# Kernel tuning notes

Hardware: AMD Instinct MI355X
Metric: run time of the kernel (lower is better)

The kernel has to match this reference:

```python
import jax, jax.numpy as jnp
import numpy as np

N_NODES = 50000
N_EDGES = 800000
F = 53
B = 128
H = 4


def _p(key, shape, scale=0.1):
    return jax.random.normal(key, shape, dtype=jnp.float32) * scale


def setup_inputs() -> dict:
    key = jax.random.key(0)
    ks = jax.random.split(key, 40)
    inp = {
        'x': jax.random.normal(ks[0], (N_NODES, F), dtype=jnp.float32),
        'edge_index': jax.random.randint(ks[1], (2, N_EDGES), 0, N_NODES),
        'batch': jnp.sort(jax.random.randint(ks[2], (N_NODES,), 0, B)),
        # GATConv(53 -> 53, heads=4)
        'gat_w': _p(ks[3], (F, H * F)),
        'gat_att_src': _p(ks[4], (H, F)),
        'gat_att_dst': _p(ks[5], (H, F)),
        'gat_bias': _p(ks[6], (H * F,)),
        # GINConv MLP: 53 -> 106 -> 106
        'gin_w1': _p(ks[7], (F, 2 * F)), 'gin_b1': _p(ks[8], (2 * F,)),
        'gin_w2': _p(ks[9], (2 * F, 2 * F)), 'gin_b2': _p(ks[10], (2 * F,)),
        # EdgeConv MLP: 106 -> 106 -> 106
        'ec_w1': _p(ks[11], (2 * F, 2 * F)), 'ec_b1': _p(ks[12], (2 * F,)),
        'ec_w2': _p(ks[13], (2 * F, 2 * F)), 'ec_b2': _p(ks[14], (2 * F,)),
        # per-branch heads
        'fg1_w': _p(ks[15], (4 * F, 256)), 'fg1_b': _p(ks[16], (256,)),
        'fg2_w': _p(ks[17], (256, 128)), 'fg2_b': _p(ks[18], (128,)),
        'fg3_w': _p(ks[19], (2 * F, 256)), 'fg3_b': _p(ks[20], (256,)),
        'fg4_w': _p(ks[21], (256, 128)), 'fg4_b': _p(ks[22], (128,)),
        'fg5_w': _p(ks[23], (2 * F, 256)), 'fg5_b': _p(ks[24], (256,)),
        'fg6_w': _p(ks[25], (256, 128)), 'fg6_b': _p(ks[26], (128,)),
        # final MLP
        'fc1_w': _p(ks[27], (384, 128)), 'fc1_b': _p(ks[28], (128,)),
        'fc2_w': _p(ks[29], (128, 64)), 'fc2_b': _p(ks[30], (64,)),
        'out_w': _p(ks[31], (64, 1)), 'out_b': _p(ks[32], (1,)),
    }
    return inp


def _gat(x, src, dst, w, a_src, a_dst, bias):
    # PyG GATConv with add_self_loops=True, negative_slope=0.2, concat heads
    n = x.shape[0]
    loop = jnp.arange(n)
    s = jnp.concatenate([src, loop])
    d = jnp.concatenate([dst, loop])
    xh = (x @ w).reshape(n, H, F)                      # [N,H,F]
    al_s = jnp.einsum('nhf,hf->nh', xh, a_src)         # [N,H]
    al_d = jnp.einsum('nhf,hf->nh', xh, a_dst)
    e = jax.nn.leaky_relu(al_s[s] + al_d[d], 0.2)      # [E2,H]
    m = jax.ops.segment_max(e, d, num_segments=n)
    ex = jnp.exp(e - m[d])
    z = jax.ops.segment_sum(ex, d, num_segments=n)
    alpha = ex / (z[d] + 1e-16)                        # softmax over in-edges
    msg = xh[s] * alpha[:, :, None]                    # [E2,H,F]
    out = jax.ops.segment_sum(msg, d, num_segments=n)
    return out.reshape(n, H * F) + bias


def _gin(x, src, dst, w1, b1, w2, b2):
    # PyG GINConv, eps=0: nn(x + sum_j x_j)
    n = x.shape[0]
    agg = jax.ops.segment_sum(x[src], dst, num_segments=n)
    h = x + agg
    return jax.nn.relu(h @ w1 + b1) @ w2 + b2


def _edgeconv(x, src, dst, w1, b1, w2, b2):
    # PyG EdgeConv: max_j nn([x_i, x_j - x_i]) at target i
    n = x.shape[0]
    xi = x[dst]
    feat = jnp.concatenate([xi, x[src] - xi], axis=-1)  # [E,2F]
    h = jax.nn.relu(feat @ w1 + b1) @ w2 + b2
    out = jax.ops.segment_max(h, dst, num_segments=n)
    return jnp.where(jnp.isfinite(out), out, 0.0)       # empty segments -> 0


def _gep(x, batch):
    # global mean pool per graph
    s = jax.ops.segment_sum(x, batch, num_segments=B)
    cnt = jax.ops.segment_sum(jnp.ones((x.shape[0],), x.dtype), batch, num_segments=B)
    return s / jnp.maximum(cnt, 1.0)[:, None]


def reference(x, edge_index, batch,
              gat_w, gat_att_src, gat_att_dst, gat_bias,
              gin_w1, gin_b1, gin_w2, gin_b2,
              ec_w1, ec_b1, ec_w2, ec_b2,
              fg1_w, fg1_b, fg2_w, fg2_b, fg3_w, fg3_b,
              fg4_w, fg4_b, fg5_w, fg5_b, fg6_w, fg6_b,
              fc1_w, fc1_b, fc2_w, fc2_b, out_w, out_b):
    relu = jax.nn.relu
    src, dst = edge_index[0], edge_index[1]

    xt = relu(_gat(x, src, dst, gat_w, gat_att_src, gat_att_dst, gat_bias))
    xt = _gep(xt, batch)
    xt = relu(xt @ fg1_w + fg1_b)
    xt = relu(xt @ fg2_w + fg2_b)

    xt2 = relu(_gin(x, src, dst, gin_w1, gin_b1, gin_w2, gin_b2))
    xt2 = _gep(xt2, batch)
    xt2 = relu(xt2 @ fg3_w + fg3_b)
    xt2 = relu(xt2 @ fg4_w + fg4_b)

    xt3 = relu(_edgeconv(x, src, dst, ec_w1, ec_b1, ec_w2, ec_b2))
    xt3 = _gep(xt3, batch)
    xt3 = relu(xt3 @ fg5_w + fg5_b)
    xt3 = relu(xt3 @ fg6_w + fg6_b)

    h = jnp.concatenate([xt, xt2, xt3], axis=1)         # [B,384]
    h = relu(h @ fc1_w + fc1_b)
    h = relu(h @ fc2_w + fc2_b)
    return jax.nn.sigmoid(h @ out_w + out_b)            # [B,1]
```

## Files before the change

kernel.cpp:

```cpp
#include <hip/hip_runtime.h>
#include <hip/hip_bf16.h>
#include <math.h>

#define N_NODES 50000
#define N_EDGES 800000
#define FDIM 53
#define BATCH 128
#define HF 212
#define F2 106
#define POOLW 424
#define PSTR 32
#define ECS 128
#define A4P 256

typedef __attribute__((ext_vector_type(8))) short short8;
typedef __attribute__((ext_vector_type(4))) float f32x4;

__device__ __forceinline__ float leaky02(float x){ return x >= 0.f ? x : 0.2f * x; }

__device__ __forceinline__ short f2bf(float x) {
  unsigned u = __float_as_uint(x);
  unsigned r = (u + 0x7fffu + ((u >> 16) & 1u)) >> 16;
  return (short)r;
}
__device__ __forceinline__ float bf2f(short b) {
  return __uint_as_float(((unsigned)(unsigned short)b) << 16);
}
__device__ __forceinline__ unsigned pk2(float a, float b) {
  union { __hip_bfloat162 h; unsigned u; } c;
  c.h = __float22bfloat162_rn(make_float2(a, b));
  return c.u;
}
__device__ __forceinline__ void ldsbar() {
  __builtin_amdgcn_s_waitcnt(0xC07F);
  __builtin_amdgcn_s_barrier();
}

#define SEG_CAL 424
#define SEG_WGT (4*56*64)
#define SEG_WUV (2*112*256)
#define SEG_WG1 (112*128)
#define SEG_WG2 (112*128)
#define PREP_TOT (SEG_CAL + SEG_WGT + SEG_WUV + SEG_WG1 + SEG_WG2)
__global__ void k_prep(const float* __restrict__ gat_w, const float* __restrict__ asrc,
                       const float* __restrict__ adst, const float* __restrict__ ec_w1,
                       const float* __restrict__ gin_w1, const float* __restrict__ gin_w2,
                       float* __restrict__ cAl, short* __restrict__ Wgt,
                       short* __restrict__ Wuv, short* __restrict__ Wg1,
                       short* __restrict__ Wg2) {
  int idx = blockIdx.x * blockDim.x + threadIdx.x;
  if (idx < SEG_CAL) {
    int k = idx >> 3, r = idx & 7, sd = r >> 2, h = r & 3;
    const float* av = sd ? adst : asrc;
    float acc = 0.f;
    for (int f = 0; f < FDIM; ++f)
      acc += gat_w[k * HF + h * FDIM + f] * av[h * FDIM + f];
    cAl[idx] = acc;
    return;
  }
  idx -= SEG_CAL;
  if (idx < SEG_WGT) {
    int h = idx / (56 * 64), rem = idx % (56 * 64);
    int n = rem >> 6, kk = rem & 63;
    Wgt[idx] = (kk < FDIM && n < FDIM) ? f2bf(gat_w[kk * HF + h * FDIM + n]) : (short)0;
    return;
  }
  idx -= SEG_WGT;
  if (idx < SEG_WUV) {
    int c = idx / (112 * 256), rem = idx % (112 * 256);
    int n = rem >> 8, kk = rem & 255, ks = kk & 63;
    float w = 0.f;
    if (ks < FDIM && n < F2)
      w = (c == 0) ? ec_w1[ks * F2 + n] - ec_w1[(FDIM + ks) * F2 + n]
                   : ec_w1[(FDIM + ks) * F2 + n];
    short hv = f2bf(w);
    Wuv[idx] = (kk < 128) ? hv : f2bf(w - bf2f(hv));
    return;
  }
  idx -= SEG_WUV;
  if (idx < SEG_WG1) {
    int n = idx >> 7, kk = idx & 127, ks = kk & 63;
    Wg1[idx] = (ks < FDIM && n < F2) ? f2bf(gin_w1[ks * F2 + n]) : (short)0;
    return;
  }
  idx -= SEG_WG1;
  if (idx < SEG_WG2) {
    int n = idx >> 7, kk = idx & 127;
    Wg2[idx] = (kk < F2 && n < F2) ? f2bf(gin_w2[kk * F2 + n]) : (short)0;
  }
}

__global__ __launch_bounds__(256) void k_xsplit(
    const float* __restrict__ x, const float* __restrict__ cAl,
    short* __restrict__ xbhl, float* __restrict__ alS, float* __restrict__ alD) {
  int wid = threadIdx.x >> 6, lane = threadIdx.x & 63;
  int i = blockIdx.x * 4 + wid;
  if (i >= N_NODES) return;
  float v = (lane < FDIM) ? x[(size_t)i * FDIM + lane] : 0.f;
  short hi = f2bf(v);
  xbhl[(size_t)i * 128 + lane] = hi;
  xbhl[(size_t)i * 128 + 64 + lane] = f2bf(v - bf2f(hi));
  float out = 0.f;
#pragma unroll
  for (int j = 0; j < 8; j++) {
    float p = (lane < FDIM) ? v * cAl[lane * 8 + j] : 0.f;
#pragma unroll
    for (int off = 32; off >= 1; off >>= 1) p += __shfl_xor(p, off);
    if (lane == j) out = p;
  }
  if (lane < 4) alS[i * 4 + lane] = out;
  else if (lane < 8) alD[i * 4 + (lane - 4)] = out;
}

__global__ __launch_bounds__(256) void k_uv(
    const short* __restrict__ xbhl, const short* __restrict__ Wuv,
    const float* __restrict__ ec_b1,
    short* __restrict__ Ub, short* __restrict__ Vb) {
  int bid = blockIdx.x;
  int nb = bid >> 1, c = bid & 1;
  int m0 = nb * 64;
  int t = threadIdx.x;
  const int lane = t & 63, wid = t >> 6;
  const int n16 = lane & 15, quad = lane >> 4;
  const int mrow0 = wid * 16;
  const size_t abase = (size_t)(m0 + mrow0 + n16) * 128;
  short8 a[4];
#pragma unroll
  for (int f = 0; f < 4; f++)
    a[f] = *(const short8*)(xbhl + abase + f * 32 + quad * 8);
  const short* Bw = Wuv + (size_t)c * 112 * 256;
  short* Ob = c ? Vb : Ub;
#pragma unroll
  for (int nt = 0; nt < 7; nt++) {
    f32x4 acc = {0.f, 0.f, 0.f, 0.f};
#pragma unroll
    for (int f = 0; f < 8; f++) {
      short8 bf = *(const short8*)(Bw + (nt * 16 + n16) * 256 + f * 32 + quad * 8);
      acc = __builtin_amdgcn_mfma_f32_16x16x32_bf16(a[f & 3], bf, acc, 0, 0, 0);
    }
    int jn = nt * 16 + n16;
    if (jn < F2) {
      float bj = c ? 0.f : ec_b1[jn];
#pragma unroll
      for (int r = 0; r < 4; r++) {
        int gm = m0 + mrow0 + quad * 4 + r;
        if (gm < N_NODES) Ob[(size_t)gm * ECS + jn] = f2bf(acc[r] + bj);
      }
    }
  }
}

#define SCAN_BLOCKS ((N_NODES + 255) / 256)

__global__ void k_hist(const int* __restrict__ ei, int* __restrict__ histP) {
  int t = blockIdx.x * blockDim.x + threadIdx.x;
  if (t < N_EDGES) atomicAdd(&histP[ei[N_EDGES + t] << 5], 1);
}

__global__ __launch_bounds__(256) void k_scan1(const int* __restrict__ histP,
                                               const int* __restrict__ batch,
                                               int* __restrict__ rp, int* __restrict__ bsum,
                                               int* __restrict__ start) {
  __shared__ int buf[256];
  int tid = threadIdx.x;
  int idx = blockIdx.x * 256 + tid;
  int v = (idx < N_NODES) ? histP[idx << 5] : 0;
  buf[tid] = v;
  __syncthreads();
  for (int off = 1; off < 256; off <<= 1) {
    int t2 = (tid >= off) ? buf[tid - off] : 0;
    __syncthreads();
    buf[tid] += t2;
    __syncthreads();
  }
  if (idx < N_NODES) rp[idx] = buf[tid] - v;
  if (tid == 255) bsum[blockIdx.x] = buf[255];
  if (idx < N_NODES) {
    int b = batch[idx];
    if (idx == 0)
      for (int g = 0; g <= b; g++) start[g] = 0;
    int bn = (idx + 1 < N_NODES) ? batch[idx + 1] : BATCH;
    for (int g = b + 1; g <= bn; g++) start[g] = idx + 1;
  }
}

__global__ __launch_bounds__(256) void k_scan3(const int* __restrict__ bsum,
                                               int* __restrict__ rp, int* __restrict__ histP) {
  __shared__ int buf[256];
  int tid = threadIdx.x;
  int v = (tid < SCAN_BLOCKS) ? bsum[tid] : 0;
  buf[tid] = v;
  __syncthreads();
  for (int off = 1; off < 256; off <<= 1) {
    int t2 = (tid >= off) ? buf[tid - off] : 0;
    __syncthreads();
    buf[tid] += t2;
    __syncthreads();
  }
  int boff = (blockIdx.x == 0) ? 0 : buf[blockIdx.x - 1];
  int idx = blockIdx.x * 256 + tid;
  if (idx < N_NODES) {
    int o = rp[idx] + boff;
    rp[idx] = o;
    histP[idx << 5] = o;
  }
  if (idx == 0) rp[N_NODES] = N_EDGES;
}

__global__ void k_scatter(const int* __restrict__ ei, int* __restrict__ histP,
                          int* __restrict__ colidx) {
  int e = blockIdx.x * blockDim.x + threadIdx.x;
  if (e >= N_EDGES) return;
  int d = ei[N_EDGES + e];
  int pos = atomicAdd(&histP[d << 5], 1);
  colidx[pos] = ei[e];
}

#define GCH 20
__global__ __launch_bounds__(256) void k_gatgin(
    const short* __restrict__ xbhl, const float* __restrict__ alS, const float* __restrict__ alD,
    const int* __restrict__ rp, const int* __restrict__ colidx,
    short* __restrict__ agg4, short* __restrict__ aggb) {
  int wid = threadIdx.x >> 6, lane = threadIdx.x & 63;
  bool fa = lane < FDIM;
  int i0 = blockIdx.x * GCH;
  int iend = min(i0 + GCH, N_NODES);
  __shared__ int rpG[GCH + 1];
  __shared__ int sL[4][64];
  __shared__ float4 eL[4][64];
  {
    int t = threadIdx.x, nn = iend - i0;
    if (t <= nn) rpG[t] = rp[i0 + t];
  }
  __syncthreads();
  for (int i = i0 + wid; i < iend; i += 4) {
    int base = rpG[i - i0], deg = rpG[i - i0 + 1] - base;
    float4 adv = *(const float4*)(alD + (size_t)i * 4);
    float4 asv = *(const float4*)(alS + (size_t)i * 4);
    float aldi[4] = {adv.x, adv.y, adv.z, adv.w};
    float exs[4];
    exs[0] = __expf(leaky02(asv.x + aldi[0]));
    exs[1] = __expf(leaky02(asv.y + aldi[1]));
    exs[2] = __expf(leaky02(asv.z + aldi[2]));
    exs[3] = __expf(leaky02(asv.w + aldi[3]));
    float xiv = fa ? bf2f(xbhl[(size_t)i * 128 + lane]) : 0.f;
    float ag0 = exs[0] * xiv, ag1 = exs[1] * xiv, ag2 = exs[2] * xiv, ag3 = exs[3] * xiv;
    float ax = xiv;
    float zl[4] = {0.f, 0.f, 0.f, 0.f};

    for (int c0 = 0; c0 < deg; c0 += 64) {
      int cn = min(64, deg - c0);
      int s = 0;
      float ex0 = 0.f, ex1 = 0.f, ex2 = 0.f, ex3 = 0.f;
      if (lane < cn) {
        s = colidx[base + c0 + lane];
        float4 av = *(const float4*)(alS + (size_t)s * 4);
        ex0 = __expf(leaky02(av.x + aldi[0]));
        ex1 = __expf(leaky02(av.y + aldi[1]));
        ex2 = __expf(leaky02(av.z + aldi[2]));
        ex3 = __expf(leaky02(av.w + aldi[3]));
        zl[0] += ex0; zl[1] += ex1; zl[2] += ex2; zl[3] += ex3;
      }
      sL[wid][lane] = s;
      eL[wid][lane] = make_float4(ex0, ex1, ex2, ex3);
      for (int jj = 0; jj < cn; jj += 4) {
        int4 s4 = *(const int4*)&sL[wid][jj];
        int sj[4] = {s4.x, s4.y, s4.z, s4.w};
        float4 e0 = eL[wid][jj + 0];
        float4 e1 = eL[wid][jj + 1];
        float4 e2 = eL[wid][jj + 2];
        float4 e3 = eL[wid][jj + 3];
        float xg[4];
#pragma unroll
        for (int q = 0; q < 4; q++)
          xg[q] = fa ? bf2f(xbhl[(size_t)sj[q] * 128 + lane]) : 0.f;
        ag0 += e0.x * xg[0] + e1.x * xg[1] + e2.x * xg[2] + e3.x * xg[3];
        ag1 += e0.y * xg[0] + e1.y * xg[1] + e2.y * xg[2] + e3.y * xg[3];
        ag2 += e0.z * xg[0] + e1.z * xg[1] + e2.z * xg[2] + e3.z * xg[3];
        ag3 += e0.w * xg[0] + e1.w * xg[1] + e2.w * xg[2] + e3.w * xg[3];
#pragma unroll
        for (int q = 0; q < 4; q++)
          if (jj + q < cn) ax += xg[q];
      }
    }
#pragma unroll
    for (int off = 32; off >= 1; off >>= 1)
#pragma unroll
      for (int h = 0; h < 4; h++) zl[h] += __shfl_xor(zl[h], off);
    {
      float z0 = zl[0] + exs[0] + 1e-16f;
      float z1 = zl[1] + exs[1] + 1e-16f;
      float z2 = zl[2] + exs[2] + 1e-16f;
      float z3 = zl[3] + exs[3] + 1e-16f;
      short* ar = agg4 + (size_t)i * A4P;
      ar[0 * 64 + lane] = fa ? f2bf(ag0 / z0) : (short)0;
      ar[1 * 64 + lane] = fa ? f2bf(ag1 / z1) : (short)0;
      ar[2 * 64 + lane] = fa ? f2bf(ag2 / z2) : (short)0;
      ar[3 * 64 + lane] = fa ? f2bf(ag3 / z3) : (short)0;
      float axv = fa ? ax : 0.f;
      short hi = f2bf(axv);
      float lov = axv - bf2f(hi);
      short* br = aggb + (size_t)i * 128;
      br[lane]      = fa ? hi : (short)0;
      br[64 + lane] = fa ? f2bf(lov) : (short)0;
    }
  }
}

__global__ __launch_bounds__(256) void k_gt(
    const short* __restrict__ agg4, const short* __restrict__ Wgt,
    const float* __restrict__ gat_b, const int* __restrict__ batch,
    float* __restrict__ pooled) {
  __shared__ float psum[4 * 224];
  __shared__ int batL[64];
  int m0 = blockIdx.x * 64;
  int t = threadIdx.x;
  for (int idx = t; idx < 4 * 224; idx += 256) psum[idx] = 0.f;
  if (t < 64) batL[t] = batch[min(m0 + t, N_NODES - 1)];
  __syncthreads();
  const int lane = t & 63, wid = t >> 6;
  const int n16 = lane & 15, quad = lane >> 4;
  const int mrow0 = wid * 16;
  const int bmin = batL[0];
  const bool uni = (batL[0] == batL[63]);
  const size_t abase = (size_t)(m0 + mrow0 + n16) * A4P;
#pragma unroll
  for (int h = 0; h < 4; h++) {
    short8 af0 = *(const short8*)(agg4 + abase + h * 64 + quad * 8);
    short8 af1 = *(const short8*)(agg4 + abase + h * 64 + 32 + quad * 8);
#pragma unroll
    for (int nt = 0; nt < 4; nt++) {
      short8 b0 = *(const short8*)(Wgt + (h * 56 + nt * 16 + n16) * 64 + quad * 8);
      short8 b1 = *(const short8*)(Wgt + (h * 56 + nt * 16 + n16) * 64 + 32 + quad * 8);
      f32x4 acc = {0.f, 0.f, 0.f, 0.f};
      acc = __builtin_amdgcn_mfma_f32_16x16x32_bf16(af0, b0, acc, 0, 0, 0);
      acc = __builtin_amdgcn_mfma_f32_16x16x32_bf16(af1, b1, acc, 0, 0, 0);
      int jn = nt * 16 + n16;
      bool jv = jn < FDIM;
      float bj = jv ? gat_b[h * FDIM + jn] : 0.f;
      if (uni) {
        float s = 0.f;
#pragma unroll
        for (int r = 0; r < 4; r++) {
          int gm = m0 + mrow0 + quad * 4 + r;
          if (gm < N_NODES) s += fmaxf(acc[r] + bj, 0.f);
        }
        s += __shfl_xor(s, 16);
        s += __shfl_xor(s, 32);
        if (quad == 0 && jv && s != 0.f) atomicAdd(&psum[h * 56 + jn], s);
      } else {
        float pj = 0.f; int curb = -1;
#pragma unroll
        for (int r = 0; r < 4; r++) {
          int lm = mrow0 + quad * 4 + r;
          int gm = m0 + lm;
          if (gm < N_NODES) {
            float o = fmaxf(acc[r] + bj, 0.f);
            int b = batL[lm];
            if (b != curb) {
              if (curb >= 0 && jv) {
                int slot = curb - bmin;
                if (slot >= 0 && slot < 4) atomicAdd(&psum[slot * 224 + h * 56 + jn], pj);
                else atomicAdd(&pooled[(size_t)curb * POOLW + h * FDIM + jn], pj);
              }
              curb = b; pj = o;
            } else {
              pj += o;
            }
          }
        }
        if (curb >= 0 && jv) {
          int slot = curb - bmin;
          if (slot >= 0 && slot < 4) atomicAdd(&psum[slot * 224 + h * 56 + jn], pj);
          else atomicAdd(&pooled[(size_t)curb * POOLW + h * FDIM + jn], pj);
        }
      }
    }
  }
  __syncthreads();
  for (int idx = t; idx < 4 * 224; idx += 256) {
    int slot = idx / 224, c = idx % 224;
    int h = c / 56, jn = c % 56;
    float v = psum[idx];
    int b = bmin + slot;
    if (jn < FDIM && b < BATCH && v != 0.f)
      atomicAdd(&pooled[(size_t)b * POOLW + h * FDIM + jn], v);
  }
}

#define H1S 132
__global__ __launch_bounds__(256) void k_ginm(
    const short* __restrict__ aggb, const short* __restrict__ Wg1,
    const short* __restrict__ Wg2,
    const float* __restrict__ b1, const float* __restrict__ b2,
    const int* __restrict__ batch, float* __restrict__ pooled) {
  __shared__ short h1hi[64 * H1S];
  __shared__ short h1lo[64 * H1S];
  __shared__ float psum[4 * 112];
  __shared__ int batL[64];
  int m0 = blockIdx.x * 64;
  int t = threadIdx.x;
  for (int idx = t; idx < 4 * 112; idx += 256) psum[idx] = 0.f;
  if (t < 64) batL[t] = batch[min(m0 + t, N_NODES - 1)];
  for (int idx = t; idx < 64 * H1S / 2; idx += 256) {
    ((int*)h1hi)[idx] = 0;
    ((int*)h1lo)[idx] = 0;
  }
  __syncthreads();
  const int lane = t & 63, wid = t >> 6;
  const int n16 = lane & 15, quad = lane >> 4;
  const int mrow0 = wid * 16;
  const int bmin = batL[0];
  const bool uni = (batL[0] == batL[63]);
  {
    const size_t abase = (size_t)(m0 + mrow0 + n16) * 128;
    short8 a[4];
#pragma unroll
    for (int f = 0; f < 4; f++)
      a[f] = *(const short8*)(aggb + abase + f * 32 + quad * 8);
#pragma unroll
    for (int nt = 0; nt < 7; nt++) {
      f32x4 acc = {0.f, 0.f, 0.f, 0.f};
#pragma unroll
      for (int f = 0; f < 4; f++) {
        short8 bf = *(const short8*)(Wg1 + (nt * 16 + n16) * 128 + f * 32 + quad * 8);
        acc = __builtin_amdgcn_mfma_f32_16x16x32_bf16(a[f], bf, acc, 0, 0, 0);
      }
      int jn = nt * 16 + n16;
      if (jn < F2) {
        float bj = b1[jn];
#pragma unroll
        for (int r = 0; r < 4; r++) {
          int row = mrow0 + quad * 4 + r;
          float v = fmaxf(acc[r] + bj, 0.f);
          short hi = f2bf(v);
          h1hi[row * H1S + jn] = hi;
          h1lo[row * H1S + jn] = f2bf(v - bf2f(hi));
        }
      }
    }
  }
  __syncthreads();
  short8 ah[4], al[4];
#pragma unroll
  for (int f = 0; f < 4; f++) {
    ah[f] = *(const short8*)&h1hi[(mrow0 + n16) * H1S + f * 32 + quad * 8];
    al[f] = *(const short8*)&h1lo[(mrow0 + n16) * H1S + f * 32 + quad * 8];
  }
#pragma unroll
  for (int nt = 0; nt < 7; nt++) {
    f32x4 acc = {0.f, 0.f, 0.f, 0.f};
#pragma unroll
    for (int f = 0; f < 4; f++) {
      short8 bf = *(const short8*)(Wg2 + (nt * 16 + n16) * 128 + f * 32 + quad * 8);
      acc = __builtin_amdgcn_mfma_f32_16x16x32_bf16(ah[f], bf, acc, 0, 0, 0);
      acc = __builtin_amdgcn_mfma_f32_16x16x32_bf16(al[f], bf, acc, 0, 0, 0);
    }
    int jn = nt * 16 + n16;
    bool jv = jn < F2;
    float bj = jv ? b2[jn] : 0.f;
    if (uni) {
      float s = 0.f;
#pragma unroll
      for (int r = 0; r < 4; r++) {
        int gm = m0 + mrow0 + quad * 4 + r;
        if (gm < N_NODES) s += fmaxf(acc[r] + bj, 0.f);
      }
      s += __shfl_xor(s, 16);
      s += __shfl_xor(s, 32);
      if (quad == 0 && jv && s != 0.f) atomicAdd(&psum[jn], s);
    } else {
      float pj = 0.f; int curb = -1;
#pragma unroll
      for (int r = 0; r < 4; r++) {
        int lm = mrow0 + quad * 4 + r;
        int gm = m0 + lm;
        if (gm < N_NODES) {
          float o = fmaxf(acc[r] + bj, 0.f);
          int b = batL[lm];
          if (b != curb) {
            if (curb >= 0 && jv) {
              int slot = curb - bmin;
              if (slot >= 0 && slot < 4) atomicAdd(&psum[slot * 112 + jn], pj);
              else atomicAdd(&pooled[(size_t)curb * POOLW + HF + jn], pj);
            }
            curb = b; pj = o;
          } else {
            pj += o;
          }
        }
      }
      if (curb >= 0 && jv) {
        int slot = curb - bmin;
        if (slot >= 0 && slot < 4) atomicAdd(&psum[slot * 112 + jn], pj);
        else atomicAdd(&pooled[(size_t)curb * POOLW + HF + jn], pj);
      }
    }
  }
  __syncthreads();
  for (int idx = t; idx < 4 * 112; idx += 256) {
    int slot = idx / 112, n = idx % 112;
    float v = psum[idx];
    int b = bmin + slot;
    if (n < F2 && b < BATCH && v != 0.f)
      atomicAdd(&pooled[(size_t)b * POOLW + HF + n], v);
  }
}

#define ECH 25
__global__ __launch_bounds__(256) void k_ec(
    const short* __restrict__ Ub, const short* __restrict__ Vb,
    const float* __restrict__ w2, const float* __restrict__ b2,
    const int* __restrict__ rp, const int* __restrict__ colidx,
    const int* __restrict__ batch, float* __restrict__ pooled) {
  const int t = threadIdx.x;
  const int lane = t & 63, wid = t >> 6;
  const int n16 = lane & 15, quad = lane >> 4;
  const int nt = (wid == 3) ? 1 : 2;

  const int i0 = blockIdx.x * ECH;
  const int iend = min(i0 + ECH, N_NODES);
  const int nn = iend - i0;

  __shared__ int rpL[ECH + 1];
  __shared__ int batL[ECH];

  short8 Bh[2][4];
  for (int tt = 0; tt < 2; tt++) {
    int ucol = (wid * 2 + tt) * 16 + n16;
    for (int kc = 0; kc < 4; kc++) {
      short8 vh;
#pragma unroll
      for (int jv = 0; jv < 8; jv++) {
        int kk = kc * 32 + quad * 8 + jv;
        float w = (ucol < F2 && kk < F2) ? w2[kk * F2 + ucol] : 0.f;
        vh[jv] = f2bf(w);
      }
      Bh[tt][kc] = vh;
    }
  }
  float b2v[2];
#pragma unroll
  for (int tt = 0; tt < 2; tt++) {
    int u = (wid * 2 + tt) * 16 + n16;
    b2v[tt] = (u < F2) ? b2[u] : 0.f;
  }

  if (t <= nn) rpL[t] = rp[i0 + t];
  if (t < nn) batL[t] = batch[i0 + t];
  __syncthreads();

  __shared__ short hs[2][16 * 16 * 8];
  union SU { short8 s; unsigned u[4]; };
  const int es = t & 15, kg = t >> 4;
  const int k0 = kg * 8;

  float sm0 = 0.f, sm1 = 0.f;
  int curb = -1;
  const int u0 = (wid * 2) * 16 + n16;
  const int u1 = (wid * 2 + 1) * 16 + n16;

  auto advance = [&](int& ii, int& ttb, int& bb, int& dd) -> bool {
    ttb++;
    if (ttb * 16 < dd) return true;
    ttb = 0;
    for (ii = ii + 1; ii < iend; ii++) {
      bb = rpL[ii - i0]; dd = rpL[ii - i0 + 1] - bb;
      if (dd > 0) return true;
    }
    return false;
  };

  int i = i0, tb = 0, base = 0, deg = 0;
  bool have = false;
  for (; i < iend; i++) {
    base = rpL[i - i0]; deg = rpL[i - i0 + 1] - base;
    if (deg > 0) { have = true; break; }
  }
  short8 pu8{}, pv8{};
  int i1 = i, tb1 = 0, base1 = base, deg1 = deg;
  bool have1 = false;
  int sc = 0;
  if (have) {
    pu8 = *(const short8*)(Ub + (size_t)i * ECS + k0);
    int s0 = colidx[base + ((es < deg) ? es : 0)];
    pv8 = *(const short8*)(Vb + (size_t)s0 * ECS + k0);
    have1 = advance(i1, tb1, base1, deg1);
    if (have1) {
      int eg = tb1 * 16 + es;
      sc = colidx[base1 + ((eg < deg1) ? eg : 0)];
    }
  }

  float Uc[8];
  float vmax0 = -1e30f, vmax1 = -1e30f;
  int parity = 0;
  while (have) {
    if (tb == 0) {
#pragma unroll
      for (int j = 0; j < 8; j++) Uc[j] = bf2f(pu8[j]);
    }
    SU w;
#pragma unroll
    for (int p = 0; p < 4; p++) {
      bool kv = (k0 + 2 * p) < F2;
      float h0 = kv ? fmaxf(Uc[2 * p]     + bf2f(pv8[2 * p]),     0.f) : 0.f;
      float h1 = kv ? fmaxf(Uc[2 * p + 1] + bf2f(pv8[2 * p + 1]), 0.f) : 0.f;
      w.u[p] = pk2(h0, h1);
    }
    *(short8*)&hs[parity][(kg * 16 + es) * 8] = w.s;

    int i2 = i1, tb2 = tb1, base2 = base1, deg2 = deg1;
    bool have2 = false;
    int scN = 0;
    if (have1) {
      if (tb1 == 0) pu8 = *(const short8*)(Ub + (size_t)i1 * ECS + k0);
      pv8 = *(const short8*)(Vb + (size_t)sc * ECS + k0);
      have2 = advance(i2, tb2, base2, deg2);
      if (have2) {
        int eg2 = tb2 * 16 + es;
        scN = colidx[base2 + ((eg2 < deg2) ? eg2 : 0)];
      }
    }

    ldsbar();
    f32x4 a0 = {0.f, 0.f, 0.f, 0.f}, a1 = {0.f, 0.f, 0.f, 0.f};
#pragma unroll
    for (int kc = 0; kc < 4; kc++) {
      short8 af = *(const short8*)&hs[parity][((kc * 4 + quad) * 16 + n16) * 8];
      a0 = __builtin_amdgcn_mfma_f32_16x16x32_bf16(af, Bh[0][kc], a0, 0, 0, 0);
      if (nt > 1)
        a1 = __builtin_amdgcn_mfma_f32_16x16x32_bf16(af, Bh[1][kc], a1, 0, 0, 0);
    }
#pragma unroll
    for (int r = 0; r < 4; r++) {
      int er = tb * 16 + quad * 4 + r;
      if (er < deg) { vmax0 = fmaxf(vmax0, a0[r]); vmax1 = fmaxf(vmax1, a1[r]); }
    }
    if (!have1 || i1 != i) {
      vmax0 = fmaxf(vmax0, __shfl_xor(vmax0, 16));
      vmax0 = fmaxf(vmax0, __shfl_xor(vmax0, 32));
      vmax1 = fmaxf(vmax1, __shfl_xor(vmax1, 16));
      vmax1 = fmaxf(vmax1, __shfl_xor(vmax1, 32));
      float o0 = fmaxf(vmax0 + b2v[0], 0.f);
      float o1 = fmaxf(vmax1 + b2v[1], 0.f);
      int b = batL[i - i0];
      if (b != curb) {
        if (curb >= 0 && quad == 0) {
          float* pg = pooled + (size_t)curb * POOLW + HF + F2;
          if (u0 < F2) atomicAdd(&pg[u0], sm0);
          if (nt > 1 && u1 < F2) atomicAdd(&pg[u1], sm1);
        }
        curb = b; sm0 = o0; sm1 = o1;
      } else {
        sm0 += o0; sm1 += o1;
      }
      vmax0 = -1e30f; vmax1 = -1e30f;
    }
    i = i1; tb = tb1; base = base1; deg = deg1; have = have1;
    i1 = i2; tb1 = tb2; base1 = base2; deg1 = deg2; have1 = have2;
    sc = scN;
    parity ^= 1;
  }
  if (curb >= 0 && quad == 0) {
    float* pg = pooled + (size_t)curb * POOLW + HF + F2;
    if (u0 < F2) atomicAdd(&pg[u0], sm0);
    if (nt > 1 && u1 < F2) atomicAdd(&pg[u1], sm1);
  }
}

__global__ __launch_bounds__(256) void k_heads(
    const float* __restrict__ pooled, const int* __restrict__ start,
    const float* __restrict__ fg1_w, const float* __restrict__ fg1_b,
    const float* __restrict__ fg2_w, const float* __restrict__ fg2_b,
    const float* __restrict__ fg3_w, const float* __restrict__ fg3_b,
    const float* __restrict__ fg4_w, const float* __restrict__ fg4_b,
    const float* __restrict__ fg5_w, const float* __restrict__ fg5_b,
    const float* __restrict__ fg6_w, const float* __restrict__ fg6_b,
    const float* __restrict__ fc1_w, const float* __restrict__ fc1_b,
    const float* __restrict__ fc2_w, const float* __restrict__ fc2_b,
    const float* __restrict__ out_w, const float* __restrict__ out_b,
    float* __restrict__ out) {
  int g = blockIdx.x, t = threadIdx.x;
  __shared__ float in[POOLW];
  __shared__ float mid[256];
  __shared__ float cat[384];
  __shared__ float h1[128];
  __shared__ float h2[64];
  float c = fmaxf((float)(start[g + 1] - start[g]), 1.f);
  for (int idx = t; idx < POOLW; idx += 256)
    in[idx] = pooled[(size_t)g * POOLW + idx] / c;
  __syncthreads();
  const float* w1s[3] = {fg1_w, fg3_w, fg5_w};
  const float* b1s[3] = {fg1_b, fg3_b, fg5_b};
  const float* w2s[3] = {fg2_w, fg4_w, fg6_w};
  const float* b2s[3] = {fg2_b, fg4_b, fg6_b};
  const int off[4] = {0, HF, HF + F2, POOLW};
  for (int br = 0; br < 3; br++) {
    int kin = off[br + 1] - off[br];
    const float* iv = &in[off[br]];
    float a = b1s[br][t];
    const float* W = w1s[br];
    for (int k = 0; k < kin; k++) a += iv[k] * W[k * 256 + t];
    mid[t] = fmaxf(a, 0.f);
    __syncthreads();
    if (t < 128) {
      float b = b2s[br][t];
      const float* W2 = w2s[br];
      for (int k = 0; k < 256; k++) b += mid[k] * W2[k * 128 + t];
      cat[br * 128 + t] = fmaxf(b, 0.f);
    }
    __syncthreads();
  }
  if (t < 128) {
    float a = fc1_b[t];
    for (int k = 0; k < 384; k++) a += cat[k] * fc1_w[k * 128 + t];
    h1[t] = fmaxf(a, 0.f);
  }
  __syncthreads();
  if (t < 64) {
    float a = fc2_b[t];
    for (int k = 0; k < 128; k++) a += h1[k] * fc2_w[k * 64 + t];
    h2[t] = fmaxf(a, 0.f);
  }
  __syncthreads();
  if (t == 0) {
    float a = out_b[0];
    for (int k = 0; k < 64; k++) a += h2[k] * out_w[k];
    out[g] = 1.f / (1.f + __expf(-a));
  }
}

extern "C" void kernel_launch(void* const* d_in, const int* in_sizes, int n_in,
                              void* d_out, int out_size, void* d_ws, size_t ws_size,
                              hipStream_t stream) {
  const float* x      = (const float*)d_in[0];
  const int*   ei     = (const int*)d_in[1];
  const int*   batch  = (const int*)d_in[2];
  const float* gat_w  = (const float*)d_in[3];
  const float* asrc   = (const float*)d_in[4];
  const float* adst   = (const float*)d_in[5];
  const float* gat_b  = (const float*)d_in[6];
  const float* gin_w1 = (const float*)d_in[7];
  const float* gin_b1 = (const float*)d_in[8];
  const float* gin_w2 = (const float*)d_in[9];
  const float* gin_b2 = (const float*)d_in[10];
  const float* ec_w1  = (const float*)d_in[11];
  const float* ec_b1  = (const float*)d_in[12];
  const float* ec_w2  = (const float*)d_in[13];
  const float* ec_b2  = (const float*)d_in[14];
  const float* fg1_w = (const float*)d_in[15]; const float* fg1_b = (const float*)d_in[16];
  const float* fg2_w = (const float*)d_in[17]; const float* fg2_b = (const float*)d_in[18];
  const float* fg3_w = (const float*)d_in[19]; const float* fg3_b = (const float*)d_in[20];
  const float* fg4_w = (const float*)d_in[21]; const float* fg4_b = (const float*)d_in[22];
  const float* fg5_w = (const float*)d_in[23]; const float* fg5_b = (const float*)d_in[24];
  const float* fg6_w = (const float*)d_in[25]; const float* fg6_b = (const float*)d_in[26];
  const float* fc1_w = (const float*)d_in[27]; const float* fc1_b = (const float*)d_in[28];
  const float* fc2_w = (const float*)d_in[29]; const float* fc2_b = (const float*)d_in[30];
  const float* out_w = (const float*)d_in[31]; const float* out_b = (const float*)d_in[32];
  float* out = (float*)d_out;

  char* ws = (char*)d_ws;
  size_t off = 0;
  auto alloc = [&](size_t bytes) -> void* {
    void* p = ws + off;
    off = (off + bytes + 255) & ~(size_t)255;
    return p;
  };
  size_t zoff0 = off;
  int*   histP  = (int*)alloc((size_t)N_NODES * PSTR * sizeof(int));
  float* pooled = (float*)alloc((size_t)BATCH * POOLW * sizeof(float));
  size_t zbytes = off - zoff0;
  int*   rp     = (int*)alloc((N_NODES + 1) * sizeof(int));
  int*   start  = (int*)alloc((BATCH + 1) * sizeof(int));
  int*   bsum   = (int*)alloc(256 * sizeof(int));
  int*   colidx = (int*)alloc(N_EDGES * sizeof(int));
  short* xbhl   = (short*)alloc((size_t)(N_NODES + 64) * 128 * sizeof(short));
  float* alS    = (float*)alloc((size_t)N_NODES * 4 * sizeof(float));
  float* alD    = (float*)alloc((size_t)N_NODES * 4 * sizeof(float));
  short* Ubuf   = (short*)alloc((size_t)N_NODES * ECS * sizeof(short));
  short* Vbuf   = (short*)alloc((size_t)N_NODES * ECS * sizeof(short));
  short* agg4   = (short*)alloc((size_t)(N_NODES + 64) * A4P * sizeof(short));
  short* aggb   = (short*)alloc((size_t)(N_NODES + 64) * 128 * sizeof(short));
  float* cAl    = (float*)alloc(SEG_CAL * sizeof(float));
  short* Wgt    = (short*)alloc(SEG_WGT * sizeof(short));
  short* Wuv    = (short*)alloc(SEG_WUV * sizeof(short));
  short* Wg1    = (short*)alloc(SEG_WG1 * sizeof(short));
  short* Wg2    = (short*)alloc(SEG_WG2 * sizeof(short));
  (void)ws_size; (void)in_sizes; (void)n_in; (void)out_size;

  hipMemsetAsync(ws + zoff0, 0, zbytes, stream);

  k_prep<<<(PREP_TOT + 255) / 256, 256, 0, stream>>>(gat_w, asrc, adst, ec_w1,
                                                     gin_w1, gin_w2,
                                                     cAl, Wgt, Wuv, Wg1, Wg2);
  k_xsplit<<<(N_NODES + 3) / 4, 256, 0, stream>>>(x, cAl, xbhl, alS, alD);
  k_uv<<<((N_NODES + 63) / 64) * 2, 256, 0, stream>>>(xbhl, Wuv, ec_b1, Ubuf, Vbuf);
  k_hist<<<(N_EDGES + 255) / 256, 256, 0, stream>>>(ei, histP);
  k_scan1<<<SCAN_BLOCKS, 256, 0, stream>>>(histP, batch, rp, bsum, start);
  k_scan3<<<SCAN_BLOCKS, 256, 0, stream>>>(bsum, rp, histP);
  k_scatter<<<(N_EDGES + 255) / 256, 256, 0, stream>>>(ei, histP, colidx);

  k_gatgin<<<(N_NODES + GCH - 1) / GCH, 256, 0, stream>>>(xbhl, alS, alD, rp, colidx,
                                                          agg4, aggb);
  k_ec<<<(N_NODES + ECH - 1) / ECH, 256, 0, stream>>>(Ubuf, Vbuf, ec_w2, ec_b2, rp, colidx, batch, pooled);
  k_gt<<<(N_NODES + 63) / 64, 256, 0, stream>>>(agg4, Wgt, gat_b, batch, pooled);
  k_ginm<<<(N_NODES + 63) / 64, 256, 0, stream>>>(aggb, Wg1, Wg2, gin_b1, gin_b2,
                                                  batch, pooled);

  k_heads<<<BATCH, 256, 0, stream>>>(pooled, start,
                                     fg1_w, fg1_b, fg2_w, fg2_b, fg3_w, fg3_b,
                                     fg4_w, fg4_b, fg5_w, fg5_b, fg6_w, fg6_b,
                                     fc1_w, fc1_b, fc2_w, fc2_b, out_w, out_b, out);
}
```

Baseline: 614.2 us.

## Fold GAT attention logits into UV MFMA and merge GAT/GIN post kernels

The GAT attention projections (x·W·a_src, x·W·a_dst) are appended as an extra 16-column tile of the U-side weight matrix, so the existing MFMA pass in k_uv produces alS/alD. This removes the per-node shuffle reductions in k_xsplit and the separate cAl precompute. The k_gt and k_ginm kernels are fused into one k_post2 kernel, saving a launch and sharing the batch/index setup. The cost is one extra MFMA tile per U block, attention logits computed in split-bf16 rather than fp32, and higher LDS use per block in the fused kernel, which may reduce occupancy.

```diff
diff --git a/kernel.cpp b/kernel.cpp
--- a/kernel.cpp
+++ b/kernel.cpp
@@ -36,29 +36,17 @@
   __builtin_amdgcn_s_barrier();
 }
 
-#define SEG_CAL 424
 #define SEG_WGT (4*56*64)
-#define SEG_WUV (2*112*256)
+#define SEG_WUV (2*128*256)
 #define SEG_WG1 (112*128)
 #define SEG_WG2 (112*128)
-#define PREP_TOT (SEG_CAL + SEG_WGT + SEG_WUV + SEG_WG1 + SEG_WG2)
+#define PREP_TOT (SEG_WGT + SEG_WUV + SEG_WG1 + SEG_WG2)
 __global__ void k_prep(const float* __restrict__ gat_w, const float* __restrict__ asrc,
                        const float* __restrict__ adst, const float* __restrict__ ec_w1,
                        const float* __restrict__ gin_w1, const float* __restrict__ gin_w2,
-                       float* __restrict__ cAl, short* __restrict__ Wgt,
-                       short* __restrict__ Wuv, short* __restrict__ Wg1,
-                       short* __restrict__ Wg2) {
+                       short* __restrict__ Wgt, short* __restrict__ Wuv,
+                       short* __restrict__ Wg1, short* __restrict__ Wg2) {
   int idx = blockIdx.x * blockDim.x + threadIdx.x;
-  if (idx < SEG_CAL) {
-    int k = idx >> 3, r = idx & 7, sd = r >> 2, h = r & 3;
-    const float* av = sd ? adst : asrc;
-    float acc = 0.f;
-    for (int f = 0; f < FDIM; ++f)
-      acc += gat_w[k * HF + h * FDIM + f] * av[h * FDIM + f];
-    cAl[idx] = acc;
-    return;
-  }
-  idx -= SEG_CAL;
   if (idx < SEG_WGT) {
     int h = idx / (56 * 64), rem = idx % (56 * 64);
     int n = rem >> 6, kk = rem & 63;
@@ -67,12 +55,25 @@
   }
   idx -= SEG_WGT;
   if (idx < SEG_WUV) {
-    int c = idx / (112 * 256), rem = idx % (112 * 256);
+    int c = idx / (128 * 256), rem = idx % (128 * 256);
     int n = rem >> 8, kk = rem & 255, ks = kk & 63;
     float w = 0.f;
-    if (ks < FDIM && n < F2)
-      w = (c == 0) ? ec_w1[ks * F2 + n] - ec_w1[(FDIM + ks) * F2 + n]
-                   : ec_w1[(FDIM + ks) * F2 + n];
+    if (ks < FDIM) {
+      if (c == 0) {
+        if (n < F2) {
+          w = ec_w1[ks * F2 + n] - ec_w1[(FDIM + ks) * F2 + n];
+        } else if (n >= 112 && n < 120) {
+          int j = n - 112, sd = j >> 2, h = j & 3;
+          const float* av = sd ? adst : asrc;
+          float acc = 0.f;
+          for (int f = 0; f < FDIM; ++f)
+            acc += gat_w[ks * HF + h * FDIM + f] * av[h * FDIM + f];
+          w = acc;
+        }
+      } else {
+        if (n < F2) w = ec_w1[(FDIM + ks) * F2 + n];
+      }
+    }
     short hv = f2bf(w);
     Wuv[idx] = (kk < 128) ? hv : f2bf(w - bf2f(hv));
     return;
@@ -91,8 +92,7 @@
 }
 
 __global__ __launch_bounds__(256) void k_xsplit(
-    const float* __restrict__ x, const float* __restrict__ cAl,
-    short* __restrict__ xbhl, float* __restrict__ alS, float* __restrict__ alD) {
+    const float* __restrict__ x, short* __restrict__ xbhl) {
   int wid = threadIdx.x >> 6, lane = threadIdx.x & 63;
   int i = blockIdx.x * 4 + wid;
   if (i >= N_NODES) return;
@@ -100,22 +100,13 @@
   short hi = f2bf(v);
   xbhl[(size_t)i * 128 + lane] = hi;
   xbhl[(size_t)i * 128 + 64 + lane] = f2bf(v - bf2f(hi));
-  float out = 0.f;
-#pragma unroll
-  for (int j = 0; j < 8; j++) {
-    float p = (lane < FDIM) ? v * cAl[lane * 8 + j] : 0.f;
-#pragma unroll
-    for (int off = 32; off >= 1; off >>= 1) p += __shfl_xor(p, off);
-    if (lane == j) out = p;
-  }
-  if (lane < 4) alS[i * 4 + lane] = out;
-  else if (lane < 8) alD[i * 4 + (lane - 4)] = out;
 }
 
 __global__ __launch_bounds__(256) void k_uv(
     const short* __restrict__ xbhl, const short* __restrict__ Wuv,
     const float* __restrict__ ec_b1,
-    short* __restrict__ Ub, short* __restrict__ Vb) {
+    short* __restrict__ Ub, short* __restrict__ Vb,
+    float* __restrict__ alS, float* __restrict__ alD) {
   int bid = blockIdx.x;
   int nb = bid >> 1, c = bid & 1;
   int m0 = nb * 64;
@@ -128,10 +119,10 @@
 #pragma unroll
   for (int f = 0; f < 4; f++)
     a[f] = *(const short8*)(xbhl + abase + f * 32 + quad * 8);
-  const short* Bw = Wuv + (size_t)c * 112 * 256;
+  const short* Bw = Wuv + (size_t)c * 128 * 256;
   short* Ob = c ? Vb : Ub;
-#pragma unroll
-  for (int nt = 0; nt < 7; nt++) {
+  const int ntmax = (c == 0) ? 8 : 7;
+  for (int nt = 0; nt < ntmax; nt++) {
     f32x4 acc = {0.f, 0.f, 0.f, 0.f};
 #pragma unroll
     for (int f = 0; f < 8; f++) {
@@ -139,12 +130,26 @@
       acc = __builtin_amdgcn_mfma_f32_16x16x32_bf16(a[f & 3], bf, acc, 0, 0, 0);
     }
     int jn = nt * 16 + n16;
-    if (jn < F2) {
-      float bj = c ? 0.f : ec_b1[jn];
-#pragma unroll
-      for (int r = 0; r < 4; r++) {
-        int gm = m0 + mrow0 + quad * 4 + r;
-        if (gm < N_NODES) Ob[(size_t)gm * ECS + jn] = f2bf(acc[r] + bj);
+    if (nt < 7) {
+      if (jn < F2) {
+        float bj = c ? 0.f : ec_b1[jn];
+#pragma unroll
+        for (int r = 0; r < 4; r++) {
+          int gm = m0 + mrow0 + quad * 4 + r;
+          if (gm < N_NODES) Ob[(size_t)gm * ECS + jn] = f2bf(acc[r] + bj);
+        }
+      }
+    } else {
+      int j = n16;
+      if (j < 8) {
+#pragma unroll
+        for (int r = 0; r < 4; r++) {
+          int gm = m0 + mrow0 + quad * 4 + r;
+          if (gm < N_NODES) {
+            if (j < 4) alS[gm * 4 + j] = acc[r];
+            else       alD[gm * 4 + (j - 4)] = acc[r];
+          }
+        }
       }
     }
   }
@@ -307,111 +312,92 @@
   }
 }
 
-__global__ __launch_bounds__(256) void k_gt(
+#define H1S 132
+__global__ __launch_bounds__(256) void k_post2(
     const short* __restrict__ agg4, const short* __restrict__ Wgt,
-    const float* __restrict__ gat_b, const int* __restrict__ batch,
-    float* __restrict__ pooled) {
-  __shared__ float psum[4 * 224];
+    const float* __restrict__ gat_b,
+    const short* __restrict__ aggb, const short* __restrict__ Wg1,
+    const short* __restrict__ Wg2,
+    const float* __restrict__ b1, const float* __restrict__ b2,
+    const int* __restrict__ batch, float* __restrict__ pooled) {
+  __shared__ float psumG[4 * 224];
+  __shared__ short h1hi[64 * H1S];
+  __shared__ short h1lo[64 * H1S];
+  __shared__ float psumN[4 * 112];
   __shared__ int batL[64];
   int m0 = blockIdx.x * 64;
   int t = threadIdx.x;
-  for (int idx = t; idx < 4 * 224; idx += 256) psum[idx] = 0.f;
+  for (int idx = t; idx < 4 * 224; idx += 256) psumG[idx] = 0.f;
+  for (int idx = t; idx < 4 * 112; idx += 256) psumN[idx] = 0.f;
   if (t < 64) batL[t] = batch[min(m0 + t, N_NODES - 1)];
+  for (int idx = t; idx < 64 * H1S / 2; idx += 256) {
+    ((int*)h1hi)[idx] = 0;
+    ((int*)h1lo)[idx] = 0;
+  }
   __syncthreads();
   const int lane = t & 63, wid = t >> 6;
   const int n16 = lane & 15, quad = lane >> 4;
   const int mrow0 = wid * 16;
   const int bmin = batL[0];
   const bool uni = (batL[0] == batL[63]);
-  const size_t abase = (size_t)(m0 + mrow0 + n16) * A4P;
-#pragma unroll
-  for (int h = 0; h < 4; h++) {
-    short8 af0 = *(const short8*)(agg4 + abase + h * 64 + quad * 8);
-    short8 af1 = *(const short8*)(agg4 + abase + h * 64 + 32 + quad * 8);
-#pragma unroll
-    for (int nt = 0; nt < 4; nt++) {
-      short8 b0 = *(const short8*)(Wgt + (h * 56 + nt * 16 + n16) * 64 + quad * 8);
-      short8 b1 = *(const short8*)(Wgt + (h * 56 + nt * 16 + n16) * 64 + 32 + quad * 8);
-      f32x4 acc = {0.f, 0.f, 0.f, 0.f};
-      acc = __builtin_amdgcn_mfma_f32_16x16x32_bf16(af0, b0, acc, 0, 0, 0);
-      acc = __builtin_amdgcn_mfma_f32_16x16x32_bf16(af1, b1, acc, 0, 0, 0);
-      int jn = nt * 16 + n16;
-      bool jv = jn < FDIM;
-      float bj = jv ? gat_b[h * FDIM + jn] : 0.f;
-      if (uni) {
-        float s = 0.f;
-#pragma unroll
-        for (int r = 0; r < 4; r++) {
-          int gm = m0 + mrow0 + quad * 4 + r;
-          if (gm < N_NODES) s += fmaxf(acc[r] + bj, 0.f);
-        }
-        s += __shfl_xor(s, 16);
-        s += __shfl_xor(s, 32);
-        if (quad == 0 && jv && s != 0.f) atomicAdd(&psum[h * 56 + jn], s);
-      } else {
-        float pj = 0.f; int curb = -1;
-#pragma unroll
-        for (int r = 0; r < 4; r++) {
-          int lm = mrow0 + quad * 4 + r;
-          int gm = m0 + lm;
-          if (gm < N_NODES) {
-            float o = fmaxf(acc[r] + bj, 0.f);
-            int b = batL[lm];
-            if (b != curb) {
-              if (curb >= 0 && jv) {
-                int slot = curb - bmin;
-                if (slot >= 0 && slot < 4) atomicAdd(&psum[slot * 224 + h * 56 + jn], pj);
-                else atomicAdd(&pooled[(size_t)curb * POOLW + h * FDIM + jn], pj);
+
+  {
+    const size_t abase = (size_t)(m0 + mrow0 + n16) * A4P;
+#pragma unroll
+    for (int h = 0; h < 4; h++) {
+      short8 af0 = *(const short8*)(agg4 + abase + h * 64 + quad * 8);
+      short8 af1 = *(const short8*)(agg4 + abase + h * 64 + 32 + quad * 8);
+#pragma unroll
+      for (int nt = 0; nt < 4; nt++) {
+        short8 b0 = *(const short8*)(Wgt + (h * 56 + nt * 16 + n16) * 64 + quad * 8);
+        short8 b1f = *(const short8*)(Wgt + (h * 56 + nt * 16 + n16) * 64 + 32 + quad * 8);
+        f32x4 acc = {0.f, 0.f, 0.f, 0.f};
+        acc = __builtin_amdgcn_mfma_f32_16x16x32_bf16(af0, b0, acc, 0, 0, 0);
+        acc = __builtin_amdgcn_mfma_f32_16x16x32_bf16(af1, b1f, acc, 0, 0, 0);
+        int jn = nt * 16 + n16;
+        bool jv = jn < FDIM;
+        float bj = jv ? gat_b[h * FDIM + jn] : 0.f;
+        if (uni) {
+          float s = 0.f;
+#pragma unroll
+          for (int r = 0; r < 4; r++) {
+            int gm = m0 + mrow0 + quad * 4 + r;
+            if (gm < N_NODES) s += fmaxf(acc[r] + bj, 0.f);
+          }
+          s += __shfl_xor(s, 16);
+          s += __shfl_xor(s, 32);
+          if (quad == 0 && jv && s != 0.f) atomicAdd(&psumG[h * 56 + jn], s);
+        } else {
+          float pj = 0.f; int curb = -1;
+#pragma unroll
+          for (int r = 0; r < 4; r++) {
+            int lm = mrow0 + quad * 4 + r;
+            int gm = m0 + lm;
+            if (gm < N_NODES) {
+              float o = fmaxf(acc[r] + bj, 0.f);
+              int b = batL[lm];
+              if (b != curb) {
+                if (curb >= 0 && jv) {
+                  int slot = curb - bmin;
+                  if (slot >= 0 && slot < 4) atomicAdd(&psumG[slot * 224 + h * 56 + jn], pj);
+                  else atomicAdd(&pooled[(size_t)curb * POOLW + h * FDIM + jn], pj);
+                }
+                curb = b; pj = o;
+              } else {
+                pj += o;
               }
-              curb = b; pj = o;
-            } else {
-              pj += o;
             }
           }
+          if (curb >= 0 && jv) {
+            int slot = curb - bmin;
+            if (slot >= 0 && slot < 4) atomicAdd(&psumG[slot * 224 + h * 56 + jn], pj);
+            else atomicAdd(&pooled[(size_t)curb * POOLW + h * FDIM + jn], pj);
+          }
         }
-        if (curb >= 0 && jv) {
-          int slot = curb - bmin;
-          if (slot >= 0 && slot < 4) atomicAdd(&psum[slot * 224 + h * 56 + jn], pj);
-          else atomicAdd(&pooled[(size_t)curb * POOLW + h * FDIM + jn], pj);
-        }
-      }
-    }
-  }
-  __syncthreads();
-  for (int idx = t; idx < 4 * 224; idx += 256) {
-    int slot = idx / 224, c = idx % 224;
-    int h = c / 56, jn = c % 56;
-    float v = psum[idx];
-    int b = bmin + slot;
-    if (jn < FDIM && b < BATCH && v != 0.f)
-      atomicAdd(&pooled[(size_t)b * POOLW + h * FDIM + jn], v);
-  }
-}
-
-#define H1S 132
-__global__ __launch_bounds__(256) void k_ginm(
-    const short* __restrict__ aggb, const short* __restrict__ Wg1,
-    const short* __restrict__ Wg2,
-    const float* __restrict__ b1, const float* __restrict__ b2,
-    const int* __restrict__ batch, float* __restrict__ pooled) {
-  __shared__ short h1hi[64 * H1S];
-  __shared__ short h1lo[64 * H1S];
-  __shared__ float psum[4 * 112];
-  __shared__ int batL[64];
-  int m0 = blockIdx.x * 64;
-  int t = threadIdx.x;
-  for (int idx = t; idx < 4 * 112; idx += 256) psum[idx] = 0.f;
-  if (t < 64) batL[t] = batch[min(m0 + t, N_NODES - 1)];
-  for (int idx = t; idx < 64 * H1S / 2; idx += 256) {
-    ((int*)h1hi)[idx] = 0;
-    ((int*)h1lo)[idx] = 0;
-  }
-  __syncthreads();
-  const int lane = t & 63, wid = t >> 6;
-  const int n16 = lane & 15, quad = lane >> 4;
-  const int mrow0 = wid * 16;
-  const int bmin = batL[0];
-  const bool uni = (batL[0] == batL[63]);
+      }
+    }
+  }
+
   {
     const size_t abase = (size_t)(m0 + mrow0 + n16) * 128;
     short8 a[4];
@@ -441,6 +427,16 @@
     }
   }
   __syncthreads();
+
+  for (int idx = t; idx < 4 * 224; idx += 256) {
+    int slot = idx / 224, c = idx % 224;
+    int h = c / 56, jn = c % 56;
+    float v = psumG[idx];
+    int b = bmin + slot;
+    if (jn < FDIM && b < BATCH && v != 0.f)
+      atomicAdd(&pooled[(size_t)b * POOLW + h * FDIM + jn], v);
+  }
+
   short8 ah[4], al[4];
 #pragma unroll
   for (int f = 0; f < 4; f++) {
@@ -468,7 +464,7 @@
       }
       s += __shfl_xor(s, 16);
       s += __shfl_xor(s, 32);
-      if (quad == 0 && jv && s != 0.f) atomicAdd(&psum[jn], s);
+      if (quad == 0 && jv && s != 0.f) atomicAdd(&psumN[jn], s);
     } else {
       float pj = 0.f; int curb = -1;
 #pragma unroll
@@ -481,7 +477,7 @@
           if (b != curb) {
             if (curb >= 0 && jv) {
               int slot = curb - bmin;
-              if (slot >= 0 && slot < 4) atomicAdd(&psum[slot * 112 + jn], pj);
+              if (slot >= 0 && slot < 4) atomicAdd(&psumN[slot * 112 + jn], pj);
               else atomicAdd(&pooled[(size_t)curb * POOLW + HF + jn], pj);
             }
             curb = b; pj = o;
@@ -492,7 +488,7 @@
       }
       if (curb >= 0 && jv) {
         int slot = curb - bmin;
-        if (slot >= 0 && slot < 4) atomicAdd(&psum[slot * 112 + jn], pj);
+        if (slot >= 0 && slot < 4) atomicAdd(&psumN[slot * 112 + jn], pj);
         else atomicAdd(&pooled[(size_t)curb * POOLW + HF + jn], pj);
       }
     }
@@ -500,7 +496,7 @@
   __syncthreads();
   for (int idx = t; idx < 4 * 112; idx += 256) {
     int slot = idx / 112, n = idx % 112;
-    float v = psum[idx];
+    float v = psumN[idx];
     int b = bmin + slot;
     if (n < F2 && b < BATCH && v != 0.f)
       atomicAdd(&pooled[(size_t)b * POOLW + HF + n], v);
@@ -782,7 +778,6 @@
   short* Vbuf   = (short*)alloc((size_t)N_NODES * ECS * sizeof(short));
   short* agg4   = (short*)alloc((size_t)(N_NODES + 64) * A4P * sizeof(short));
   short* aggb   = (short*)alloc((size_t)(N_NODES + 64) * 128 * sizeof(short));
-  float* cAl    = (float*)alloc(SEG_CAL * sizeof(float));
   short* Wgt    = (short*)alloc(SEG_WGT * sizeof(short));
   short* Wuv    = (short*)alloc(SEG_WUV * sizeof(short));
   short* Wg1    = (short*)alloc(SEG_WG1 * sizeof(short));
@@ -793,9 +788,10 @@
 
   k_prep<<<(PREP_TOT + 255) / 256, 256, 0, stream>>>(gat_w, asrc, adst, ec_w1,
                                                      gin_w1, gin_w2,
-                                                     cAl, Wgt, Wuv, Wg1, Wg2);
-  k_xsplit<<<(N_NODES + 3) / 4, 256, 0, stream>>>(x, cAl, xbhl, alS, alD);
-  k_uv<<<((N_NODES + 63) / 64) * 2, 256, 0, stream>>>(xbhl, Wuv, ec_b1, Ubuf, Vbuf);
+                                                     Wgt, Wuv, Wg1, Wg2);
+  k_xsplit<<<(N_NODES + 3) / 4, 256, 0, stream>>>(x, xbhl);
+  k_uv<<<((N_NODES + 63) / 64) * 2, 256, 0, stream>>>(xbhl, Wuv, ec_b1,
+                                                      Ubuf, Vbuf, alS, alD);
   k_hist<<<(N_EDGES + 255) / 256, 256, 0, stream>>>(ei, histP);
   k_scan1<<<SCAN_BLOCKS, 256, 0, stream>>>(histP, batch, rp, bsum, start);
   k_scan3<<<SCAN_BLOCKS, 256, 0, stream>>>(bsum, rp, histP);
@@ -804,9 +800,9 @@
   k_gatgin<<<(N_NODES + GCH - 1) / GCH, 256, 0, stream>>>(xbhl, alS, alD, rp, colidx,
                                                           agg4, aggb);
   k_ec<<<(N_NODES + ECH - 1) / ECH, 256, 0, stream>>>(Ubuf, Vbuf, ec_w2, ec_b2, rp, colidx, batch, pooled);
-  k_gt<<<(N_NODES + 63) / 64, 256, 0, stream>>>(agg4, Wgt, gat_b, batch, pooled);
-  k_ginm<<<(N_NODES + 63) / 64, 256, 0, stream>>>(aggb, Wg1, Wg2, gin_b1, gin_b2,
-                                                  batch, pooled);
+  k_post2<<<(N_NODES + 63) / 64, 256, 0, stream>>>(agg4, Wgt, gat_b,
+                                                   aggb, Wg1, Wg2, gin_b1, gin_b2,
+                                                   batch, pooled);
 
   k_heads<<<BATCH, 256, 0, stream>>>(pooled, start,
                                      fg1_w, fg1_b, fg2_w, fg2_b, fg3_w, fg3_b,
```

After: 595.3 us. 1.03x faster.
